# Optimization experiments

Hardware: AMD Instinct MI355X
Metric: run time of the kernel (lower is better)

The kernel has to match this reference:

```python
import jax, jax.numpy as jnp
import numpy as np

EPS = 1e-8


def box2corners(box):
    # box: (B, N, 5) = (x, y, w, h, alpha) -> corners (B, N, 4, 2)
    x, y, w, h, alpha = (box[..., i] for i in range(5))
    x4 = jnp.asarray([0.5, -0.5, -0.5, 0.5], box.dtype) * w[..., None]   # (B,N,4)
    y4 = jnp.asarray([0.5, 0.5, -0.5, -0.5], box.dtype) * h[..., None]
    c = jnp.cos(alpha)[..., None]
    s = jnp.sin(alpha)[..., None]
    cx = x4 * c - y4 * s + x[..., None]
    cy = x4 * s + y4 * c + y[..., None]
    return jnp.stack([cx, cy], axis=-1)


def _cross2(a, b):
    return a[..., 0] * b[..., 1] - a[..., 1] * b[..., 0]


def box_intersection(corners1, corners2):
    # pairwise segment intersections of the 4 edges of each box: (B,N,16,2), mask (B,N,16)
    q1 = jnp.roll(corners1, -1, axis=2)
    q2 = jnp.roll(corners2, -1, axis=2)
    p1 = corners1[:, :, :, None, :]          # (B,N,4,1,2)
    r = (q1 - corners1)[:, :, :, None, :]    # edge dirs of box1
    p2 = corners2[:, :, None, :, :]          # (B,N,1,4,2)
    s = (q2 - corners2)[:, :, None, :, :]    # edge dirs of box2
    den = _cross2(r, s)                      # (B,N,4,4)
    dp = p2 - p1
    t = _cross2(dp, s) / (den + EPS)
    u = _cross2(dp, r) / (den + EPS)
    mask = (t > 0.0) & (t < 1.0) & (u > 0.0) & (u < 1.0)
    inter = (p1 + t[..., None] * r) * mask[..., None]
    B, N = corners1.shape[:2]
    return inter.reshape(B, N, 16, 2), mask.reshape(B, N, 16)


def box_in_box(pts, box):
    # check whether the 4 corners `pts` (B,N,4,2) lie inside rectangle `box` (B,N,4,2)
    a = box[:, :, 0:1, :]
    ab = box[:, :, 1:2, :] - a
    ad = box[:, :, 3:4, :] - a
    am = pts - a
    pab = (am * ab).sum(-1) / (ab * ab).sum(-1)
    pad = (am * ad).sum(-1) / (ad * ad).sum(-1)
    e = 1e-6
    return (pab > -e) & (pab < 1 + e) & (pad > -e) & (pad < 1 + e)


def oriented_box_intersection_2d(corners1, corners2):
    inter, inter_mask = box_intersection(corners1, corners2)
    c1_in_2 = box_in_box(corners1, corners2)
    c2_in_1 = box_in_box(corners2, corners1)
    vertices = jnp.concatenate([corners1, corners2, inter], axis=2)   # (B,N,24,2)
    mask = jnp.concatenate([c1_in_2, c2_in_1, inter_mask], axis=2)    # (B,N,24) bool
    num_valid = mask.sum(-1)                                           # (B,N) int
    mean = (vertices * mask[..., None]).sum(axis=2, keepdims=True) / \
        jnp.maximum(num_valid[..., None, None], 1).astype(vertices.dtype)
    v = (vertices - mean) * mask[..., None]   # invalid -> zero vectors
    ang = jnp.where(mask, jnp.arctan2(v[..., 1], v[..., 0]), 1e3)  # invalid pushed to end
    order = jnp.argsort(ang, axis=-1)
    vs = jnp.take_along_axis(v, order[..., None], axis=2)  # valid CCW-sorted, zeros after
    # shoelace over consecutive pairs; zero rows contribute nothing
    total = (vs[..., :-1, 0] * vs[..., 1:, 1] - vs[..., 1:, 0] * vs[..., :-1, 1]).sum(-1)
    # close the polygon: cross(v_last_valid, v_first)
    idx_last = jnp.maximum(num_valid - 1, 0)[..., None, None]
    v_last = jnp.take_along_axis(vs, jnp.broadcast_to(idx_last, (*vs.shape[:2], 1, 2)), axis=2)[:, :, 0]
    v0 = vs[:, :, 0]
    total = total + (v_last[..., 0] * v0[..., 1] - v0[..., 0] * v_last[..., 1])
    return jnp.abs(total) * 0.5, vs


def diff_iou_rotated_3d(box3d1, box3d2):
    box1 = box3d1[..., jnp.array([0, 1, 3, 4, 6])]
    box2 = box3d2[..., jnp.array([0, 1, 3, 4, 6])]
    corners1 = box2corners(box1)
    corners2 = box2corners(box2)
    inter_2d, _ = oriented_box_intersection_2d(corners1, corners2)
    zmax1 = box3d1[..., 2] + box3d1[..., 5] * 0.5
    zmin1 = box3d1[..., 2] - box3d1[..., 5] * 0.5
    zmax2 = box3d2[..., 2] + box3d2[..., 5] * 0.5
    zmin2 = box3d2[..., 2] - box3d2[..., 5] * 0.5
    z_overlap = jnp.clip(jnp.minimum(zmax1, zmax2) - jnp.maximum(zmin1, zmin2), 0.0, None)
    inter_3d = inter_2d * z_overlap
    vol1 = box3d1[..., 3] * box3d1[..., 4] * box3d1[..., 5]
    vol2 = box3d2[..., 3] * box3d2[..., 4] * box3d2[..., 5]
    union_3d = vol1 + vol2 - inter_3d
    return inter_3d / union_3d


def setup_inputs() -> dict:
    key = jax.random.key(0)
    k1, k2 = jax.random.split(key)
    N = 1_000_000
    pred = jax.random.uniform(k1, (N, 7), dtype=jnp.float32)
    target = jax.random.uniform(k2, (N, 7), dtype=jnp.float32)
    return {"pred": pred, "target": target}


def reference(pred, target):
    # RotatedIoU3DLoss(mode='iou', reduction='mean', loss_weight=1.0), weight=None
    iou = diff_iou_rotated_3d(pred[None], target[None])[0]  # (N,)
    return 1.0 * jnp.mean(1.0 - iou)
```

## Files before the change

kernel.cpp:

```cpp
#include <hip/hip_runtime.h>
#include <math.h>

__device__ __forceinline__ float frcp(float x) { return __builtin_amdgcn_rcpf(x); }

__device__ __forceinline__ float edge_area(float px, float py, float qx, float qy,
                                           float hw, float hh) {
    const float Y0 = -hh, Y1 = hh;
    float dx = qx - px, dy = qy - py;
    float lo = fmaxf(fminf(px, qx), -hw);
    float hi = fminf(fmaxf(px, qx),  hw);
    float w  = hi - lo;
    float dys = (fabsf(dy) > 1e-20f) ? dy : ((dy >= 0.f) ? 1e-20f : -1e-20f);
    float dxs = (fabsf(dx) > 1e-20f) ? dx : ((dx >= 0.f) ? 1e-20f : -1e-20f);
    float xdy = dx * frcp(dys);
    float m   = dy * frcp(dxs);
    float xa = fmaf(Y0 - py, xdy, px);
    float xb = fmaf(Y1 - py, xdy, px);
    float s0 = fminf(xa, xb), s1 = fmaxf(xa, xb);
    float u0 = fminf(fmaxf(s0, lo), hi);
    float u1 = fminf(fmaxf(s1, lo), hi);
    float yu0 = fmaf(m, u0 - px, py);
    float yu1 = fmaf(m, u1 - px, py);
    yu0 = fminf(fmaxf(yu0, Y0), Y1);
    yu1 = fminf(fmaxf(yu1, Y0), Y1);
    bool mpos = (dy >= 0.f) == (dx >= 0.f);
    float YL = mpos ? Y0 : Y1;
    float YR = mpos ? Y1 : Y0;
    float integral = YL * (u0 - lo)
                   + 0.5f * (yu0 + yu1) * (u1 - u0)
                   + YR * (hi - u1);
    float contrib = integral - Y0 * w;
    float res = (dx > 0.f) ? -contrib : contrib;
    return (w > 0.f) ? res : 0.f;
}

__device__ __forceinline__ float elem_loss(const float b1[7], const float b2[7]) {
    float x1 = b1[0], y1 = b1[1], z1 = b1[2], w1 = b1[3], h1 = b1[4], dz1 = b1[5], a1 = b1[6];
    float x2 = b2[0], y2 = b2[1], z2 = b2[2], w2 = b2[3], h2 = b2[4], dz2 = b2[5], a2 = b2[6];

    float zo = fmaxf(fminf(z1 + 0.5f * dz1, z2 + 0.5f * dz2)
                   - fmaxf(z1 - 0.5f * dz1, z2 - 0.5f * dz2), 0.0f);
    float vol1 = w1 * h1 * dz1;
    float vol2 = w2 * h2 * dz2;

    float sa = __sinf(a2), ca = __cosf(a2);
    float dxc = x1 - x2, dyc = y1 - y2;
    float tx =  dxc * ca + dyc * sa;
    float ty = -dxc * sa + dyc * ca;
    float ad = a1 - a2;
    float sd = __sinf(ad), cd = __cosf(ad);
    float hw1 = 0.5f * w1, hh1 = 0.5f * h1;
    float hw2 = 0.5f * w2, hh2 = 0.5f * h2;
    float ex = hw1 * cd, ey = hw1 * sd;
    float fx = -hh1 * sd, fy = hh1 * cd;
    float q0x = tx + ex + fx, q0y = ty + ey + fy;
    float q1x = tx - ex + fx, q1y = ty - ey + fy;
    float q2x = tx - ex - fx, q2y = ty - ey - fy;
    float q3x = tx + ex - fx, q3y = ty + ey - fy;

    float area = edge_area(q0x, q0y, q1x, q1y, hw2, hh2)
               + edge_area(q1x, q1y, q2x, q2y, hw2, hh2)
               + edge_area(q2x, q2y, q3x, q3y, hw2, hh2)
               + edge_area(q3x, q3y, q0x, q0y, hw2, hh2);
    area = fabsf(area);

    float inter3d = area * zo;
    float union3d = vol1 + vol2 - inter3d;
    return 1.0f - inter3d * frcp(union3d);
}

#define WAVES 4
#define TILES 4
#define TILE_ELEMS 128

__global__ __launch_bounds__(256) void iou3d_loss_kernel(
    const float* __restrict__ pred, const float* __restrict__ target,
    float* __restrict__ partial, int N)
{
    __shared__ float lds[WAVES][1792];
    const int lane = threadIdx.x & 63;
    const int wid  = threadIdx.x >> 6;
    const long gw  = (long)blockIdx.x * WAVES + wid;
    const long tile0 = gw * TILES;
    const long totF2 = ((long)N * 7) >> 1;

    const float2* pred2 = (const float2*)pred;
    const float2* targ2 = (const float2*)target;
    float2* ldsP = (float2*)&lds[wid][0];
    float2* ldsT = (float2*)&lds[wid][896];

    float val = 0.f;

    float2 pa[7], pb[7];
    {
        const long f2b = tile0 * 448;
        #pragma unroll
        for (int k = 0; k < 7; k++) {
            long idx = f2b + k * 64 + lane;
            bool ok = idx < totF2;
            pa[k] = ok ? pred2[idx] : make_float2(0.f, 0.f);
            pb[k] = ok ? targ2[idx] : make_float2(0.f, 0.f);
        }
    }

    #pragma unroll 1
    for (int t = 0; t < TILES; t++) {
        #pragma unroll
        for (int k = 0; k < 7; k++) {
            ldsP[k * 64 + lane] = pa[k];
            ldsT[k * 64 + lane] = pb[k];
        }
        if (t + 1 < TILES) {
            const long f2b = (tile0 + t + 1) * 448;
            #pragma unroll
            for (int k = 0; k < 7; k++) {
                long idx = f2b + k * 64 + lane;
                bool ok = idx < totF2;
                pa[k] = ok ? pred2[idx] : make_float2(0.f, 0.f);
                pb[k] = ok ? targ2[idx] : make_float2(0.f, 0.f);
            }
        }
        float af[14], bf[14];
        #pragma unroll
        for (int j = 0; j < 7; j++) {
            float2 va = ldsP[7 * lane + j];
            float2 vb = ldsT[7 * lane + j];
            af[2 * j] = va.x; af[2 * j + 1] = va.y;
            bf[2 * j] = vb.x; bf[2 * j + 1] = vb.y;
        }
        long e0 = (tile0 + t) * TILE_ELEMS + 2 * lane;
        if (e0 < N)     val += elem_loss(&af[0], &bf[0]);
        if (e0 + 1 < N) val += elem_loss(&af[7], &bf[7]);
    }

    #pragma unroll
    for (int off = 32; off > 0; off >>= 1)
        val += __shfl_down(val, off, 64);
    __shared__ float wsum[WAVES];
    if (lane == 0) wsum[wid] = val;
    __syncthreads();
    if (threadIdx.x == 0) {
        float s = 0.f;
        #pragma unroll
        for (int q = 0; q < WAVES; q++) s += wsum[q];
        partial[blockIdx.x] = s;
    }
}

__global__ __launch_bounds__(1024) void iou3d_finalize_kernel(
    const float* __restrict__ partial, float* __restrict__ out, int nb, int N)
{
    float s = 0.f;
    for (int i = threadIdx.x; i < nb; i += 1024) s += partial[i];
    #pragma unroll
    for (int off = 32; off > 0; off >>= 1)
        s += __shfl_down(s, off, 64);
    __shared__ float ws[16];
    int lane = threadIdx.x & 63, wid = threadIdx.x >> 6;
    if (lane == 0) ws[wid] = s;
    __syncthreads();
    if (threadIdx.x == 0) {
        float t = 0.f;
        #pragma unroll
        for (int q = 0; q < 16; q++) t += ws[q];
        out[0] = (float)((double)t / (double)N);
    }
}

extern "C" void kernel_launch(void* const* d_in, const int* in_sizes, int n_in,
                              void* d_out, int out_size, void* d_ws, size_t ws_size,
                              hipStream_t stream) {
    const float* pred   = (const float*)d_in[0];
    const float* target = (const float*)d_in[1];
    int N = in_sizes[0] / 7;
    float* partial = (float*)d_ws;

    long tiles = ((long)N + TILE_ELEMS - 1) / TILE_ELEMS;
    long waves = (tiles + TILES - 1) / TILES;
    int grid = (int)((waves + WAVES - 1) / WAVES);
    iou3d_loss_kernel<<<grid, 256, 0, stream>>>(pred, target, partial, N);
    iou3d_finalize_kernel<<<1, 1024, 0, stream>>>(partial, (float*)d_out, grid, N);
}
```

Baseline: 20.11 us.

## Fuse finalize reduction into main kernel via last-block atomic counter

Removes the separate finalize kernel launch. Each block now writes its partial sum, fences, and bumps an atomic counter, and the last block to arrive sums all partials and writes the mean. It also switches index arithmetic from 64-bit to 32-bit and adds an unguarded load path for full tiles. It adds a hipMemsetAsync to reset the counter, so one launch is replaced by a memset node, and the fence/atomic adds a little serialization at the tail.

```diff
diff --git a/kernel.cpp b/kernel.cpp
--- a/kernel.cpp
+++ b/kernel.cpp
@@ -73,35 +73,47 @@
 #define TILES 4
 #define TILE_ELEMS 128
 
-__global__ __launch_bounds__(256) void iou3d_loss_kernel(
+
+__global__ __launch_bounds__(256) void iou3d_fused_kernel(
     const float* __restrict__ pred, const float* __restrict__ target,
-    float* __restrict__ partial, int N)
+    float* __restrict__ partial, unsigned* __restrict__ counter,
+    float* __restrict__ out, int N, int nblocks)
 {
     __shared__ float lds[WAVES][1792];
     const int lane = threadIdx.x & 63;
     const int wid  = threadIdx.x >> 6;
-    const long gw  = (long)blockIdx.x * WAVES + wid;
-    const long tile0 = gw * TILES;
-    const long totF2 = ((long)N * 7) >> 1;
+    const int gw   = blockIdx.x * WAVES + wid;
+    const int tile0 = gw * TILES;
+    const int totF2 = (N * 7) >> 1;
 
     const float2* pred2 = (const float2*)pred;
     const float2* targ2 = (const float2*)target;
     float2* ldsP = (float2*)&lds[wid][0];
     float2* ldsT = (float2*)&lds[wid][896];
 
+    float2 pa[7], pb[7];
+
+    #define PREFETCH(TIDX) do { \
+        const int f2b_ = (TIDX) * 448; \
+        if (((TIDX) + 1) * TILE_ELEMS <= N) { \
+            _Pragma("unroll") \
+            for (int k = 0; k < 7; k++) { \
+                int idx = f2b_ + k * 64 + lane; \
+                pa[k] = pred2[idx]; pb[k] = targ2[idx]; \
+            } \
+        } else { \
+            _Pragma("unroll") \
+            for (int k = 0; k < 7; k++) { \
+                int idx = f2b_ + k * 64 + lane; \
+                bool ok = idx < totF2; \
+                pa[k] = ok ? pred2[idx] : make_float2(0.f, 0.f); \
+                pb[k] = ok ? targ2[idx] : make_float2(0.f, 0.f); \
+            } \
+        } \
+    } while (0)
+
     float val = 0.f;
-
-    float2 pa[7], pb[7];
-    {
-        const long f2b = tile0 * 448;
-        #pragma unroll
-        for (int k = 0; k < 7; k++) {
-            long idx = f2b + k * 64 + lane;
-            bool ok = idx < totF2;
-            pa[k] = ok ? pred2[idx] : make_float2(0.f, 0.f);
-            pb[k] = ok ? targ2[idx] : make_float2(0.f, 0.f);
-        }
-    }
+    PREFETCH(tile0);
 
     #pragma unroll 1
     for (int t = 0; t < TILES; t++) {
@@ -110,16 +122,7 @@
             ldsP[k * 64 + lane] = pa[k];
             ldsT[k * 64 + lane] = pb[k];
         }
-        if (t + 1 < TILES) {
-            const long f2b = (tile0 + t + 1) * 448;
-            #pragma unroll
-            for (int k = 0; k < 7; k++) {
-                long idx = f2b + k * 64 + lane;
-                bool ok = idx < totF2;
-                pa[k] = ok ? pred2[idx] : make_float2(0.f, 0.f);
-                pb[k] = ok ? targ2[idx] : make_float2(0.f, 0.f);
-            }
-        }
+        if (t + 1 < TILES) PREFETCH(tile0 + t + 1);
         float af[14], bf[14];
         #pragma unroll
         for (int j = 0; j < 7; j++) {
@@ -128,42 +131,40 @@
             af[2 * j] = va.x; af[2 * j + 1] = va.y;
             bf[2 * j] = vb.x; bf[2 * j + 1] = vb.y;
         }
-        long e0 = (tile0 + t) * TILE_ELEMS + 2 * lane;
+        int e0 = (tile0 + t) * TILE_ELEMS + 2 * lane;
         if (e0 < N)     val += elem_loss(&af[0], &bf[0]);
         if (e0 + 1 < N) val += elem_loss(&af[7], &bf[7]);
     }
+    #undef PREFETCH
 
     #pragma unroll
     for (int off = 32; off > 0; off >>= 1)
         val += __shfl_down(val, off, 64);
     __shared__ float wsum[WAVES];
+    __shared__ bool last;
     if (lane == 0) wsum[wid] = val;
     __syncthreads();
     if (threadIdx.x == 0) {
+        float s = wsum[0] + wsum[1] + wsum[2] + wsum[3];
+        partial[blockIdx.x] = s;
+        __threadfence();
+        unsigned old = atomicAdd(counter, 1u);
+        last = (old == (unsigned)(nblocks - 1));
+    }
+    __syncthreads();
+    if (last) {
+        __threadfence();
         float s = 0.f;
+        for (int i = threadIdx.x; i < nblocks; i += 256) s += partial[i];
         #pragma unroll
-        for (int q = 0; q < WAVES; q++) s += wsum[q];
-        partial[blockIdx.x] = s;
-    }
-}
-
-__global__ __launch_bounds__(1024) void iou3d_finalize_kernel(
-    const float* __restrict__ partial, float* __restrict__ out, int nb, int N)
-{
-    float s = 0.f;
-    for (int i = threadIdx.x; i < nb; i += 1024) s += partial[i];
-    #pragma unroll
-    for (int off = 32; off > 0; off >>= 1)
-        s += __shfl_down(s, off, 64);
-    __shared__ float ws[16];
-    int lane = threadIdx.x & 63, wid = threadIdx.x >> 6;
-    if (lane == 0) ws[wid] = s;
-    __syncthreads();
-    if (threadIdx.x == 0) {
-        float t = 0.f;
-        #pragma unroll
-        for (int q = 0; q < 16; q++) t += ws[q];
-        out[0] = (float)((double)t / (double)N);
+        for (int off = 32; off > 0; off >>= 1)
+            s += __shfl_down(s, off, 64);
+        if (lane == 0) wsum[wid] = s;
+        __syncthreads();
+        if (threadIdx.x == 0) {
+            float tsum = wsum[0] + wsum[1] + wsum[2] + wsum[3];
+            out[0] = (float)((double)tsum / (double)N);
+        }
     }
 }
 
@@ -173,11 +174,15 @@
     const float* pred   = (const float*)d_in[0];
     const float* target = (const float*)d_in[1];
     int N = in_sizes[0] / 7;
-    float* partial = (float*)d_ws;
+
+    float*    partial = (float*)d_ws;
+    unsigned* counter = (unsigned*)((char*)d_ws + (1 << 20));
 
     long tiles = ((long)N + TILE_ELEMS - 1) / TILE_ELEMS;
     long waves = (tiles + TILES - 1) / TILES;
     int grid = (int)((waves + WAVES - 1) / WAVES);
-    iou3d_loss_kernel<<<grid, 256, 0, stream>>>(pred, target, partial, N);
-    iou3d_finalize_kernel<<<1, 1024, 0, stream>>>(partial, (float*)d_out, grid, N);
+
+    hipMemsetAsync(counter, 0, sizeof(unsigned), stream);
+    iou3d_fused_kernel<<<grid, 256, 0, stream>>>(pred, target, partial, counter,
+                                                 (float*)d_out, N, grid);
 }
```

New measurement: 33.24 us. 1.65x slower.
